# Kernel tuning notes

Hardware: AMD Instinct MI355X
Metric: run time of the kernel (lower is better)

## Reference

```python
import jax, jax.numpy as jnp
import numpy as np

N_NODES = 100000
N_EDGES = 3200000
N_FEAT = 128
HIDDEN = 16
N_CLASSES = 10
N_GRAPHS = 512


def setup_inputs() -> dict:
    key = jax.random.key(0)
    ks = jax.random.split(key, 12)
    x = jax.random.normal(ks[0], (N_NODES, N_FEAT), dtype=jnp.float32)
    edge_index = jax.random.randint(ks[1], (2, N_EDGES), 0, N_NODES, dtype=jnp.int64)
    batch = jnp.sort(jax.random.randint(ks[2], (N_NODES,), 0, N_GRAPHS, dtype=jnp.int64))
    def glorot(k, fan_in, fan_out):
        s = jnp.sqrt(6.0 / (fan_in + fan_out)).astype(jnp.float32)
        return jax.random.uniform(k, (fan_in, fan_out), jnp.float32, -s, s)
    W1 = glorot(ks[3], N_FEAT, HIDDEN); b1 = jnp.zeros((HIDDEN,), jnp.float32)
    W2 = glorot(ks[4], HIDDEN, HIDDEN); b2 = jnp.zeros((HIDDEN,), jnp.float32)
    W3 = glorot(ks[5], HIDDEN, HIDDEN); b3 = jnp.zeros((HIDDEN,), jnp.float32)
    Wlin = glorot(ks[6], HIDDEN, N_CLASSES)
    blin = jnp.zeros((N_CLASSES,), jnp.float32)
    return {"x": x, "edge_index": edge_index, "batch": batch,
            "W1": W1, "b1": b1, "W2": W2, "b2": b2, "W3": W3, "b3": b3,
            "Wlin": Wlin, "blin": blin}


def _gcn_conv(x, W, b, src, dst, norm, n):
    # h = X W ; out[dst] += norm * h[src] ; + bias
    h = x @ W
    out = jax.ops.segment_sum(h[src] * norm[:, None], dst, num_segments=n)
    return out + b


def reference(x, edge_index, batch, W1, b1, W2, b2, W3, b3, Wlin, blin):
    n = x.shape[0]
    loop = jnp.arange(n, dtype=edge_index.dtype)
    src = jnp.concatenate([edge_index[0], loop])  # add self-loops (PyG GCNConv default)
    dst = jnp.concatenate([edge_index[1], loop])
    # symmetric degree normalization: deg over destination (incl. self-loops)
    deg = jax.ops.segment_sum(jnp.ones_like(dst, dtype=x.dtype), dst, num_segments=n)
    dinv = jnp.where(deg > 0, jax.lax.rsqrt(jnp.maximum(deg, 1.0)), 0.0)
    norm = dinv[src] * dinv[dst]  # [E+N]

    h = jax.nn.relu(_gcn_conv(x, W1, b1, src, dst, norm, n))
    h = jax.nn.relu(_gcn_conv(h, W2, b2, src, dst, norm, n))
    h = _gcn_conv(h, W3, b3, src, dst, norm, n)
    # global add pool over graphs
    pooled = jax.ops.segment_sum(h, batch, num_segments=N_GRAPHS)  # [G, hidden]
    # dropout p=0.5 is identity in eval mode
    return pooled @ Wlin + blin
```

## Files before the change

### kernel.cpp

```cpp
#include <hip/hip_runtime.h>
#include <hip/hip_fp16.h>

#define N_NODES   100000
#define N_EDGES   3200000
#define N_FEAT    128
#define HIDDEN    16
#define N_CLASSES 10
#define N_GRAPHS  512
#define NPB       256
#define NBUCKET   391
#define EPB       4096
#define PBLK      ((N_EDGES + EPB - 1) / EPB)
#define PSLACK    15872
#define CSLACK    9216


__global__ void cursor_init_kernel(int* __restrict__ cur) {
    int i = blockIdx.x * 256 + threadIdx.x;
    if (i < NBUCKET) cur[i] = i * PSLACK;
}

__global__ __launch_bounds__(512) void partition_kernel(const int* __restrict__ src,
                                                        const int* __restrict__ dst,
                                                        int* __restrict__ cur,
                                                        unsigned* __restrict__ part) {
    __shared__ int cnt[NBUCKET];
    __shared__ int lbase[NBUCKET];
    __shared__ int rk[NBUCKET];
    __shared__ int gbase[NBUCKET];
    __shared__ int s[512];
    __shared__ unsigned sorted[EPB];
    __shared__ unsigned short bb[EPB];
    __shared__ unsigned char  dl[EPB];
    int tid = threadIdx.x;
    for (int i = tid; i < NBUCKET; i += 512) cnt[i] = 0;
    __syncthreads();
    int s0 = blockIdx.x * EPB;
#pragma unroll
    for (int i = 0; i < EPB / 512; ++i) {
        int le = i * 512 + tid;
        int e  = s0 + le;
        if (e < N_EDGES) {
            int d = dst[e];
            int b = d >> 8;
            bb[le] = (unsigned short)b;
            dl[le] = (unsigned char)(d & 255);
            atomicAdd(&cnt[b], 1);
        }
    }
    __syncthreads();
    int v = (tid < NBUCKET) ? cnt[tid] : 0;
    s[tid] = v;
    __syncthreads();
    for (int off = 1; off < 512; off <<= 1) {
        int t = (tid >= off) ? s[tid - off] : 0;
        __syncthreads();
        s[tid] += t;
        __syncthreads();
    }
    if (tid < NBUCKET) {
        int lb = s[tid] - v;
        lbase[tid] = lb;
        rk[tid]    = lb;
        int cpad = (v + 15) & ~15;
        gbase[tid] = cpad ? atomicAdd(&cur[tid], cpad) : 0;
    }
    __syncthreads();
#pragma unroll
    for (int i = 0; i < EPB / 512; ++i) {
        int le = i * 512 + tid;
        int e  = s0 + le;
        if (e < N_EDGES) {
            int b = bb[le];
            int r = atomicAdd(&rk[b], 1);
            sorted[r] = (unsigned)src[e] | ((unsigned)dl[le] << 17);
        }
    }
    __syncthreads();
    int w16 = tid >> 4, l16 = tid & 15;
    for (int b = w16; b < NBUCKET; b += 32) {
        int c = cnt[b];
        if (!c) continue;
        int cpad = (c + 15) & ~15;
        int lb = lbase[b], gb = gbase[b];
        for (int j = l16; j < cpad; j += 16)
            part[gb + j] = (j < c) ? sorted[lb + j] : 0xFFFFFFFFu;
    }
}

__global__ __launch_bounds__(512) void build_csr_kernel(const unsigned* __restrict__ part,
                                                        const int* __restrict__ cur,
                                                        int2* __restrict__ rp,
                                                        float* __restrict__ dinv, int* __restrict__ csr) {
    __shared__ int ncnt[256];
    __shared__ int s[512];
    int b   = blockIdx.x;
    int tid = threadIdx.x;
    int beg = b * PSLACK, end = cur[b];
    if (tid < 256) ncnt[tid] = 0;
    __syncthreads();
    for (int j = beg + tid; j < end; j += 512) {
        unsigned r = part[j];
        if (r != 0xFFFFFFFFu) atomicAdd(&ncnt[(r >> 17) & 255], 1);
    }
    __syncthreads();
    int deg = (tid < 256) ? ncnt[tid] : 0;
    s[tid] = deg;
    __syncthreads();
    for (int off = 1; off < 512; off <<= 1) {
        int t = (tid >= off) ? s[tid - off] : 0;
        __syncthreads();
        s[tid] += t;
        __syncthreads();
    }
    int excl = s[tid] - deg;
    int cbeg = b * CSLACK;
    if (tid < 256) {
        int node = b * 256 + tid;
        if (node < N_NODES) {
            rp[node]   = make_int2(cbeg + excl, cbeg + excl + deg);
            dinv[node] = rsqrtf((float)(deg + 1));
        }
    }
    __syncthreads();
    if (tid < 256) ncnt[tid] = cbeg + excl;
    __syncthreads();
    for (int j = beg + tid; j < end; j += 512) {
        unsigned r = part[j];
        if (r != 0xFFFFFFFFu) {
            int vv = (r >> 17) & 255;
            int slot = atomicAdd(&ncnt[vv], 1);
            csr[slot] = (int)(r & 0x1FFFFu);
        }
    }
}


__device__ __forceinline__ void pack_store8(__half* outp, int idx, const float* o) {
    int4 w;
    __half2 q;
    q = __floats2half2_rn(o[0], o[1]); w.x = *(int*)&q;
    q = __floats2half2_rn(o[2], o[3]); w.y = *(int*)&q;
    q = __floats2half2_rn(o[4], o[5]); w.z = *(int*)&q;
    q = __floats2half2_rn(o[6], o[7]); w.w = *(int*)&q;
    ((int4*)outp)[idx] = w;
}

__global__ void transform_x_kernel(const float* __restrict__ x, const float* __restrict__ W,
                                   const float* __restrict__ dinv, __half* __restrict__ g) {
    __shared__ float Wl[N_FEAT * HIDDEN];
    int tid = threadIdx.x;
    for (int i = tid; i < N_FEAT * HIDDEN; i += 256) Wl[i] = W[i];
    __syncthreads();
    int v = blockIdx.x * 256 + tid;
    if (v >= N_NODES) return;
    float acc[HIDDEN];
#pragma unroll
    for (int f = 0; f < HIDDEN; ++f) acc[f] = 0.f;
    const float4* xr = (const float4*)(x + (size_t)v * N_FEAT);
#pragma unroll 4
    for (int k4 = 0; k4 < N_FEAT / 4; ++k4) {
        float4 xv = xr[k4];
        const float* wr = &Wl[k4 * 4 * HIDDEN];
#pragma unroll
        for (int f = 0; f < HIDDEN; ++f)
            acc[f] += xv.x * wr[f] + xv.y * wr[HIDDEN + f] +
                      xv.z * wr[2 * HIDDEN + f] + xv.w * wr[3 * HIDDEN + f];
    }
    float di = dinv[v];
#pragma unroll
    for (int f = 0; f < HIDDEN; ++f) acc[f] *= di;
    pack_store8(g, v * 2,     &acc[0]);
    pack_store8(g, v * 2 + 1, &acc[8]);
}

template <int MODE>
__global__ __launch_bounds__(256) void aggregate_kernel(
        const __half* __restrict__ g, const int2* __restrict__ rp,
        const int* __restrict__ csr, const float* __restrict__ dinv,
        const float* __restrict__ bias, const float* __restrict__ Wn,
        __half* __restrict__ out) {
    __shared__ float WnL[HIDDEN * HIDDEN];
    int tid  = threadIdx.x;
    if (MODE == 2) {
        if (tid < HIDDEN * HIDDEN) WnL[tid] = Wn[tid];
        __syncthreads();
    }
    int wave = tid >> 6;
    int l    = tid & 63;
    int c  = l >> 3;
    int vl = (l >> 1) & 3;
    int hh = l & 1;
    int v = blockIdx.x * 16 + wave * 4 + vl;
    int2 range = rp[v];
    int beg = range.x, end = range.y;
    const int4* g4 = (const int4*)g;
    float a0 = 0.f, a1 = 0.f, a2 = 0.f, a3 = 0.f, a4 = 0.f, a5 = 0.f, a6 = 0.f, a7 = 0.f;
#pragma unroll 4
    for (int j = beg + c; j < end; j += 8) {
        int s = csr[j];
        int4 r = g4[s * 2 + hh];
        float2 f0 = __half22float2(*(const __half2*)&r.x);
        float2 f1 = __half22float2(*(const __half2*)&r.y);
        float2 f2 = __half22float2(*(const __half2*)&r.z);
        float2 f3 = __half22float2(*(const __half2*)&r.w);
        a0 += f0.x; a1 += f0.y; a2 += f1.x; a3 += f1.y;
        a4 += f2.x; a5 += f2.y; a6 += f3.x; a7 += f3.y;
    }
    a0 += __shfl_xor(a0, 8);  a1 += __shfl_xor(a1, 8);
    a2 += __shfl_xor(a2, 8);  a3 += __shfl_xor(a3, 8);
    a4 += __shfl_xor(a4, 8);  a5 += __shfl_xor(a5, 8);
    a6 += __shfl_xor(a6, 8);  a7 += __shfl_xor(a7, 8);
    a0 += __shfl_xor(a0, 16); a1 += __shfl_xor(a1, 16);
    a2 += __shfl_xor(a2, 16); a3 += __shfl_xor(a3, 16);
    a4 += __shfl_xor(a4, 16); a5 += __shfl_xor(a5, 16);
    a6 += __shfl_xor(a6, 16); a7 += __shfl_xor(a7, 16);
    a0 += __shfl_xor(a0, 32); a1 += __shfl_xor(a1, 32);
    a2 += __shfl_xor(a2, 32); a3 += __shfl_xor(a3, 32);
    a4 += __shfl_xor(a4, 32); a5 += __shfl_xor(a5, 32);
    a6 += __shfl_xor(a6, 32); a7 += __shfl_xor(a7, 32);
    if (c == 0) {
        int4 r = g4[v * 2 + hh];
        float2 s0 = __half22float2(*(const __half2*)&r.x);
        float2 s1 = __half22float2(*(const __half2*)&r.y);
        float2 s2 = __half22float2(*(const __half2*)&r.z);
        float2 s3 = __half22float2(*(const __half2*)&r.w);
        float di = dinv[v];
        const float4* bp = (const float4*)bias;
        float4 bA = bp[hh * 2];
        float4 bB = bp[hh * 2 + 1];
        float o[8];
        o[0] = di * (a0 + s0.x) + bA.x;
        o[1] = di * (a1 + s0.y) + bA.y;
        o[2] = di * (a2 + s1.x) + bA.z;
        o[3] = di * (a3 + s1.y) + bA.w;
        o[4] = di * (a4 + s2.x) + bB.x;
        o[5] = di * (a5 + s2.y) + bB.y;
        o[6] = di * (a6 + s3.x) + bB.z;
        o[7] = di * (a7 + s3.y) + bB.w;
        if (MODE == 2) {
#pragma unroll
            for (int i = 0; i < 8; ++i) o[i] = fmaxf(o[i], 0.f);
            float pa[16];
#pragma unroll
            for (int f = 0; f < 16; ++f) pa[f] = 0.f;
            const float* wr = &WnL[hh * 8 * HIDDEN];
#pragma unroll
            for (int q = 0; q < 8; ++q) {
                float hq = o[q];
#pragma unroll
                for (int f = 0; f < 16; ++f) pa[f] += hq * wr[q * HIDDEN + f];
            }
            float o2[8];
#pragma unroll
            for (int i = 0; i < 8; ++i) {
                float lo = pa[i];
                float hi = pa[8 + i];
                float keep = hh ? hi : lo;
                float send = hh ? lo : hi;
                float recv = __shfl_xor(send, 1);
                o2[i] = di * (keep + recv);
            }
            pack_store8(out, v * 2 + hh, o2);
        } else {
            pack_store8(out, v * 2 + hh, o);
        }
    }
}


__global__ void pool_head_kernel(const __half* __restrict__ h, const int* __restrict__ batch,
                                 const float* __restrict__ Wlin, const float* __restrict__ blin,
                                 float* __restrict__ out) {
    __shared__ float red[256];
    __shared__ int bounds[2];
    int g   = blockIdx.x;
    int tid = threadIdx.x;
    if (tid < 2) {
        int target = g + tid;
        int lo = 0, hi = N_NODES;
        while (lo < hi) {
            int mid = (lo + hi) >> 1;
            if (batch[mid] < target) lo = mid + 1; else hi = mid;
        }
        bounds[tid] = lo;
    }
    __syncthreads();
    int start = bounds[0], end = bounds[1];
    int f = tid & 15, r = tid >> 4;
    float acc = 0.f;
    for (int v = start + r; v < end; v += 16)
        acc += __half2float(h[v * HIDDEN + f]);
    red[tid] = acc;
    __syncthreads();
    for (int off = 128; off >= 16; off >>= 1) {
        if (tid < off) red[tid] += red[tid + off];
        __syncthreads();
    }
    if (tid < N_CLASSES) {
        float s = blin[tid];
#pragma unroll
        for (int fe = 0; fe < HIDDEN; ++fe) s += red[fe] * Wlin[fe * N_CLASSES + tid];
        out[g * N_CLASSES + tid] = s;
    }
}


extern "C" void kernel_launch(void* const* d_in, const int* in_sizes, int n_in,
                              void* d_out, int out_size, void* d_ws, size_t ws_size,
                              hipStream_t stream) {
    const float* x     = (const float*)d_in[0];
    const int*   ei    = (const int*)d_in[1];
    const int*   src   = ei;
    const int*   dst   = ei + N_EDGES;
    const int*   batch = (const int*)d_in[2];
    const float* W1 = (const float*)d_in[3];
    const float* b1 = (const float*)d_in[4];
    const float* W2 = (const float*)d_in[5];
    const float* b2 = (const float*)d_in[6];
    const float* W3 = (const float*)d_in[7];
    const float* b3 = (const float*)d_in[8];
    const float* Wlin = (const float*)d_in[9];
    const float* blin = (const float*)d_in[10];
    float* out = (float*)d_out;

    char* w = (char*)d_ws;
    auto alloc = [&](size_t bytes) -> char* {
        char* p = w;
        w += (bytes + 255) & ~(size_t)255;
        return p;
    };
    int*    cur    = (int*)alloc((size_t)NBUCKET * 4);
    int2*   rp     = (int2*)alloc((size_t)N_NODES * 8);
    float*  dinv   = (float*)alloc((size_t)N_NODES * 4);
    __half* gA     = (__half*)alloc((size_t)N_NODES * HIDDEN * 2);
    __half* gB     = (__half*)alloc((size_t)N_NODES * HIDDEN * 2);
    __half* hA     = (__half*)alloc((size_t)N_NODES * HIDDEN * 2);
    unsigned* part = (unsigned*)alloc((size_t)NBUCKET * PSLACK * 4);
    int*    csr    = (int*)alloc((size_t)NBUCKET * CSLACK * 4);

    int nbn = (N_NODES + 255) / 256;
    int ab  = (N_NODES + 15) / 16;

    cursor_init_kernel<<<(NBUCKET + 255) / 256, 256, 0, stream>>>(cur);
    partition_kernel<<<PBLK, 512, 0, stream>>>(src, dst, cur, part);
    build_csr_kernel<<<NBUCKET, 512, 0, stream>>>(part, cur, rp, dinv, csr);

    transform_x_kernel<<<nbn, 256, 0, stream>>>(x, W1, dinv, gA);
    aggregate_kernel<2><<<ab, 256, 0, stream>>>(gA, rp, csr, dinv, b1, W2, gB);
    aggregate_kernel<2><<<ab, 256, 0, stream>>>(gB, rp, csr, dinv, b2, W3, gA);
    aggregate_kernel<0><<<ab, 256, 0, stream>>>(gA, rp, csr, dinv, b3, nullptr, hA);

    pool_head_kernel<<<N_GRAPHS, 256, 0, stream>>>(hA, batch, Wlin, blin, out);
}
```

Baseline: 270.5 us.

## Split X@W1 rows across 4 lanes with coalesced loads and packed half2 FMAs

The first-layer transform now uses four lanes per node instead of one thread per node. Each lane loads interleaved float4 chunks of the row, so the loads coalesce, and accumulates in packed half2 FMAs against a half2 copy of W held in LDS. Partial sums are combined with lane shuffles. This targets uncoalesced per-thread row loads and scalar FP32 FMA throughput, at the cost of FP16 accumulation precision over 128 features and extra shuffle work.

```diff
diff --git a/kernel.cpp b/kernel.cpp
--- a/kernel.cpp
+++ b/kernel.cpp
@@ -146,32 +146,65 @@
     ((int4*)outp)[idx] = w;
 }
 
-__global__ void transform_x_kernel(const float* __restrict__ x, const float* __restrict__ W,
-                                   const float* __restrict__ dinv, __half* __restrict__ g) {
-    __shared__ float Wl[N_FEAT * HIDDEN];
+__global__ __launch_bounds__(256) void transform_x_kernel(const float* __restrict__ x,
+                                                          const float* __restrict__ W,
+                                                          const float* __restrict__ dinv,
+                                                          __half* __restrict__ g) {
+    __shared__ __half2 Wp[1024];
     int tid = threadIdx.x;
-    for (int i = tid; i < N_FEAT * HIDDEN; i += 256) Wl[i] = W[i];
-    __syncthreads();
-    int v = blockIdx.x * 256 + tid;
-    if (v >= N_NODES) return;
-    float acc[HIDDEN];
-#pragma unroll
-    for (int f = 0; f < HIDDEN; ++f) acc[f] = 0.f;
-    const float4* xr = (const float4*)(x + (size_t)v * N_FEAT);
-#pragma unroll 4
-    for (int k4 = 0; k4 < N_FEAT / 4; ++k4) {
-        float4 xv = xr[k4];
-        const float* wr = &Wl[k4 * 4 * HIDDEN];
-#pragma unroll
-        for (int f = 0; f < HIDDEN; ++f)
-            acc[f] += xv.x * wr[f] + xv.y * wr[HIDDEN + f] +
-                      xv.z * wr[2 * HIDDEN + f] + xv.w * wr[3 * HIDDEN + f];
-    }
-    float di = dinv[v];
-#pragma unroll
-    for (int f = 0; f < HIDDEN; ++f) acc[f] *= di;
-    pack_store8(g, v * 2,     &acc[0]);
-    pack_store8(g, v * 2 + 1, &acc[8]);
+    for (int i = tid; i < 1024; i += 256) {
+        int kp = i >> 4, f = i & 15;
+        Wp[i] = __floats2half2_rn(W[(2 * kp) * HIDDEN + f], W[(2 * kp + 1) * HIDDEN + f]);
+    }
+    __syncthreads();
+    int l  = tid & 63;
+    int wv = tid >> 6;
+    int rw = l >> 2;
+    int q  = l & 3;
+    int row = blockIdx.x * 64 + wv * 16 + rw;
+    if (row >= N_NODES) return;
+    const float4* xp = (const float4*)x + (size_t)row * 32;
+    float4 xr[8];
+#pragma unroll
+    for (int s8 = 0; s8 < 8; ++s8) xr[s8] = xp[q + 4 * s8];
+    __half2 acc[16];
+    const __half2 z2 = __floats2half2_rn(0.f, 0.f);
+#pragma unroll
+    for (int f = 0; f < 16; ++f) acc[f] = z2;
+    const int4* w4 = (const int4*)Wp;
+#pragma unroll
+    for (int s8 = 0; s8 < 8; ++s8) {
+        int k4 = q + 4 * s8;
+        __half2 xp0 = __floats2half2_rn(xr[s8].x, xr[s8].y);
+        __half2 xp1 = __floats2half2_rn(xr[s8].z, xr[s8].w);
+#pragma unroll
+        for (int hf = 0; hf < 2; ++hf) {
+            int kp = 2 * k4 + hf;
+            __half2 xv = hf ? xp1 : xp0;
+#pragma unroll
+            for (int j = 0; j < 4; ++j) {
+                int4 wj = w4[kp * 4 + j];
+                const __half2* wvv = (const __half2*)&wj;
+#pragma unroll
+                for (int ff = 0; ff < 4; ++ff)
+                    acc[j * 4 + ff] = __hfma2(xv, wvv[ff], acc[j * 4 + ff]);
+            }
+        }
+    }
+    float di = dinv[row];
+    float o[16];
+#pragma unroll
+    for (int f = 0; f < 16; ++f) {
+        float2 t = __half22float2(acc[f]);
+        float sv = t.x + t.y;
+        sv += __shfl_xor(sv, 1);
+        sv += __shfl_xor(sv, 2);
+        o[f] = sv * di;
+    }
+    if (q == 0) {
+        pack_store8(g, row * 2,     &o[0]);
+        pack_store8(g, row * 2 + 1, &o[8]);
+    }
 }
 
 template <int MODE>
@@ -246,10 +279,10 @@
             for (int f = 0; f < 16; ++f) pa[f] = 0.f;
             const float* wr = &WnL[hh * 8 * HIDDEN];
 #pragma unroll
-            for (int q = 0; q < 8; ++q) {
-                float hq = o[q];
-#pragma unroll
-                for (int f = 0; f < 16; ++f) pa[f] += hq * wr[q * HIDDEN + f];
+            for (int qq = 0; qq < 8; ++qq) {
+                float hq = o[qq];
+#pragma unroll
+                for (int f = 0; f < 16; ++f) pa[f] += hq * wr[qq * HIDDEN + f];
             }
             float o2[8];
 #pragma unroll
@@ -339,14 +372,14 @@
     unsigned* part = (unsigned*)alloc((size_t)NBUCKET * PSLACK * 4);
     int*    csr    = (int*)alloc((size_t)NBUCKET * CSLACK * 4);
 
-    int nbn = (N_NODES + 255) / 256;
+    int ntx = (N_NODES + 63) / 64;
     int ab  = (N_NODES + 15) / 16;
 
     cursor_init_kernel<<<(NBUCKET + 255) / 256, 256, 0, stream>>>(cur);
     partition_kernel<<<PBLK, 512, 0, stream>>>(src, dst, cur, part);
     build_csr_kernel<<<NBUCKET, 512, 0, stream>>>(part, cur, rp, dinv, csr);
 
-    transform_x_kernel<<<nbn, 256, 0, stream>>>(x, W1, dinv, gA);
+    transform_x_kernel<<<ntx, 256, 0, stream>>>(x, W1, dinv, gA);
     aggregate_kernel<2><<<ab, 256, 0, stream>>>(gA, rp, csr, dinv, b1, W2, gB);
     aggregate_kernel<2><<<ab, 256, 0, stream>>>(gB, rp, csr, dinv, b2, W3, gA);
     aggregate_kernel<0><<<ab, 256, 0, stream>>>(gA, rp, csr, dinv, b3, nullptr, hA);
```

After: 263.7 us, median of 2. -2.5%, faster.
